# Optimization experiments

Hardware: AMD Instinct MI355X
Metric: run time of the kernel (lower is better)

## Reference

```python
import jax, jax.numpy as jnp
import numpy as np

N = 50000          # nodes
E = 800000         # edges (no self loops; self loops added in reference)
D = 128            # in_channels == out_channels (required by index_add into x)
HEADS = 1
NEG_SLOPE = 0.2
NUM_LABELS = 7


def setup_inputs() -> dict:
    key = jax.random.key(0)
    k0, k1, k2, k3, k4, k5 = jax.random.split(key, 6)
    x = jax.random.normal(k0, (N, D), dtype=jnp.float32)
    # edges guaranteed self-loop-free (remove_self_loops is then a no-op)
    src = jax.random.randint(k1, (E,), 0, N, dtype=jnp.int32)
    off = jax.random.randint(k2, (E,), 1, N, dtype=jnp.int32)
    dst = (src + off) % N
    edge_index = jnp.stack([src, dst])  # [2, E]
    node_label = jax.random.randint(k3, (N,), 0, 8, dtype=jnp.int32)  # 0 = inactive, 1..7 active
    glorot = float(np.sqrt(6.0 / (D + D)))
    weight_id = jax.random.uniform(k4, (NUM_LABELS, D, D), jnp.float32, -glorot, glorot)
    ga = float(np.sqrt(6.0 / (HEADS * 2 * D + 1)))
    att = jax.random.uniform(k5, (1, HEADS, 2 * D), jnp.float32, -ga, ga)
    return {"x": x, "edge_index": edge_index, "node_label": node_label,
            "weight_id": weight_id, "att": att}


def reference(x, edge_index, node_label, weight_id, att):
    n, d = x.shape
    # --- per-label identity transform: ox = x + W_{label-1} x for labels 1..7 ---
    y = jnp.einsum('nd,kdo->nko', x, weight_id)           # [N, 7, D]
    valid = (node_label >= 1) & (node_label <= NUM_LABELS)
    idx = jnp.clip(node_label - 1, 0, NUM_LABELS - 1)
    delta = jnp.take_along_axis(y, idx[:, None, None], axis=1)[:, 0]  # [N, D]
    ox = x + jnp.where(valid[:, None], delta, jnp.zeros_like(delta))
    # --- add self loops (input has none) ---
    loops = jnp.arange(n, dtype=edge_index.dtype)
    src = jnp.concatenate([edge_index[0], loops])
    dst = jnp.concatenate([edge_index[1], loops])
    # --- GAT message: gather, attention score, edge softmax over dst ---
    x_j = ox[src].reshape(-1, HEADS, d)                   # [Et, 1, D]
    x_i = ox[dst].reshape(-1, HEADS, d)
    alpha = (x_i * att[:, :, :d]).sum(-1) + (x_j * att[:, :, d:]).sum(-1)  # [Et, 1]
    alpha = jax.nn.leaky_relu(alpha, NEG_SLOPE)
    amax = jax.ops.segment_max(alpha, dst, num_segments=n)  # every node has a self loop
    alpha = jnp.exp(alpha - amax[dst])
    denom = jax.ops.segment_sum(alpha, dst, num_segments=n)
    alpha = alpha / (denom[dst] + 1e-16)
    # dropout p=0 (eval) -> no-op
    msg = (x_j * alpha[:, :, None]).reshape(-1, HEADS * d)  # concat=True, heads=1
    out = jax.ops.segment_sum(msg, dst, num_segments=n)     # [N, D]; bias=False
    return out
```

## Files before the change

kernel.cpp:

```cpp
#include <hip/hip_runtime.h>
#include <math.h>

#define N_NODES 50000
#define N_EDGES 800000
#define DIM 128
#define DEG_CAP 48
#define BINS ((N_NODES + 255) / 256)
#define BIN_CAP 8192
#define EA_CHUNK 3125
#define BA_BLOCKS ((N_EDGES + EA_CHUNK - 1) / EA_CHUNK)

#define LB_BLOCKS ((N_NODES + 255) / 256)
#define WT_BLOCKS ((7 * DIM * DIM + 255) / 256)
#define K1_GRID (BA_BLOCKS + LB_BLOCKS + WT_BLOCKS)

#define TR_BLOCKS 784
#define K2_GRID (BINS + TR_BLOCKS)

typedef __attribute__((ext_vector_type(8))) short short8;
typedef __attribute__((ext_vector_type(4))) float floatx4;

__device__ __forceinline__ unsigned short f2bf(float f) {
    unsigned int u = __float_as_uint(f);
    unsigned int r = (u + 0x7fff + ((u >> 16) & 1)) >> 16;
    return (unsigned short)r;
}
__device__ __forceinline__ float bf2f_lo(unsigned int v) { return __uint_as_float(v << 16); }
__device__ __forceinline__ float bf2f_hi(unsigned int v) { return __uint_as_float(v & 0xffff0000u); }

__global__ __launch_bounds__(256) void build_kernel(
        const int* __restrict__ src, const int* __restrict__ dst,
        const int* __restrict__ label, const float* __restrict__ W,
        unsigned short* __restrict__ Wt,
        int* __restrict__ bin_cur, unsigned int* __restrict__ binned,
        int* __restrict__ lab_cnt, int* __restrict__ node_list) {
    int t = threadIdx.x;
    int blk = blockIdx.x;

    if (blk < BA_BLOCKS) {
        __shared__ int hist[BINS], base_s[BINS], rank[BINS];
        for (int i = t; i < BINS; i += 256) { hist[i] = 0; rank[i] = 0; }
        __syncthreads();
        int e0 = blk * EA_CHUNK;
        int e1 = e0 + EA_CHUNK; if (e1 > N_EDGES) e1 = N_EDGES;
        for (int e = e0 + t; e < e1; e += 256) atomicAdd(&hist[dst[e] >> 8], 1);
        __syncthreads();
        for (int i = t; i < BINS; i += 256)
            base_s[i] = (hist[i] > 0) ? atomicAdd(&bin_cur[i], hist[i]) : 0;
        __syncthreads();
        for (int e = e0 + t; e < e1; e += 256) {
            int d = dst[e];
            int b = d >> 8;
            int r = atomicAdd(&rank[b], 1);
            int slot = base_s[b] + r;
            if (slot < BIN_CAP)
                binned[(size_t)b * BIN_CAP + slot] = (unsigned int)(src[e] | ((d & 255) << 16));
        }
    } else if (blk < BA_BLOCKS + LB_BLOCKS) {
        __shared__ int lcnt[8], lbase[8], lrank[8];
        int i = (blk - BA_BLOCKS) * 256 + t;
        if (t < 8) { lcnt[t] = 0; lrank[t] = 0; }
        __syncthreads();
        int b = -1;
        if (i < N_NODES) {
            int lab = label[i];
            b = (lab >= 1 && lab <= 7) ? (lab - 1) : 7;
            atomicAdd(&lcnt[b], 1);
        }
        __syncthreads();
        if (t < 8) lbase[t] = (lcnt[t] > 0) ? atomicAdd(&lab_cnt[t], lcnt[t]) : 0;
        __syncthreads();
        if (i < N_NODES) {
            int r = atomicAdd(&lrank[b], 1);
            node_list[(size_t)b * N_NODES + lbase[b] + r] = i;
        }
    } else {
        int j = (blk - BA_BLOCKS - LB_BLOCKS) * 256 + t;
        if (j < 7 * DIM * DIM) {
            int b = j >> 14;
            int d = (j >> 7) & 127;
            int c = j & 127;
            Wt[((size_t)b * DIM + c) * DIM + d] = f2bf(W[j]);
        }
    }
}

__global__ __launch_bounds__(256) void phase2_kernel(
        const float* __restrict__ x, const float* __restrict__ att,
        const int* __restrict__ lab_cnt, const int* __restrict__ node_list,
        const unsigned short* __restrict__ Wt,
        const int* __restrict__ bin_cur, const unsigned int* __restrict__ binned,
        unsigned short* __restrict__ oxh, float* __restrict__ ai, float* __restrict__ aj,
        int* __restrict__ cnt, unsigned short* __restrict__ bucket) {
    int t = threadIdx.x;
    int blk = blockIdx.x;

    if (blk < BINS) {
        __shared__ unsigned short rows[256][DEG_CAP];
        __shared__ int lcnt[256];
        int b = blk;
        int m = bin_cur[b]; if (m > BIN_CAP) m = BIN_CAP;
        const unsigned int* bp = binned + (size_t)b * BIN_CAP;

        lcnt[t] = 0;
        __syncthreads();
        for (int i = t; i < m; i += 256) {
            unsigned int v = bp[i];
            int ln = (v >> 16) & 255;
            int p = atomicAdd(&lcnt[ln], 1);
            if (p < DEG_CAP) rows[ln][p] = (unsigned short)(v & 0xFFFF);
        }
        __syncthreads();
        int n = b * 256 + t;
        if (n < N_NODES) {
            int deg = lcnt[t];
            if (deg > DEG_CAP) deg = DEG_CAP;
            cnt[n] = deg;
        }
        uint4* gdst = (uint4*)(bucket + (size_t)b * 256 * DEG_CAP);
        const uint4* lsrc = (const uint4*)rows;
        #pragma unroll
        for (int k = 0; k < (256 * DEG_CAP * 2 / 16) / 256; k++)
            gdst[t + k * 256] = lsrc[t + k * 256];
    } else {
        int wv = t >> 6;
        int lane = t & 63;
        int tile = (blk - BINS) * 4 + wv;

        int b = 0, base = 0, tcnt = 0;
        for (; b < 8; b++) {
            int c = lab_cnt[b];
            int nt = (c + 15) >> 4;
            if (tile < nt) { base = b * N_NODES + tile * 16; tcnt = c - tile * 16; break; }
            tile -= nt;
        }
        if (b == 8) return;
        if (tcnt > 16) tcnt = 16;

        int m = lane & 15;
        int quad = lane >> 4;

        floatx4 acc[8];
        #pragma unroll
        for (int nt = 0; nt < 8; nt++) acc[nt] = (floatx4){0.f, 0.f, 0.f, 0.f};

        if (b < 7) {
            int mm = (m < tcnt) ? m : 0;
            int nodeA = node_list[base + mm];
            const float* xrow = x + (size_t)nodeA * DIM;
            short8 afrag[4];
            #pragma unroll
            for (int kk = 0; kk < 4; kk++) {
                float4 f0 = *(const float4*)(xrow + kk * 32 + quad * 8);
                float4 f1 = *(const float4*)(xrow + kk * 32 + quad * 8 + 4);
                short8 a;
                a[0] = (short)f2bf(f0.x); a[1] = (short)f2bf(f0.y);
                a[2] = (short)f2bf(f0.z); a[3] = (short)f2bf(f0.w);
                a[4] = (short)f2bf(f1.x); a[5] = (short)f2bf(f1.y);
                a[6] = (short)f2bf(f1.z); a[7] = (short)f2bf(f1.w);
                afrag[kk] = a;
            }

            const unsigned short* WtB = Wt + (size_t)b * DIM * DIM;
            #pragma unroll
            for (int kk = 0; kk < 4; kk++) {
                #pragma unroll
                for (int nt = 0; nt < 8; nt++) {
                    short8 bfrag = *(const short8*)(WtB + (size_t)(nt * 16 + m) * DIM + kk * 32 + quad * 8);
                    acc[nt] = __builtin_amdgcn_mfma_f32_16x16x32_bf16(afrag[kk], bfrag, acc[nt], 0, 0, 0);
                }
            }
        }

        int nodes[4];
        #pragma unroll
        for (int r = 0; r < 4; r++) {
            int rw = quad * 4 + r;
            nodes[r] = node_list[base + ((rw < tcnt) ? rw : 0)];
        }
        float pi[4] = {0.f, 0.f, 0.f, 0.f};
        float pj[4] = {0.f, 0.f, 0.f, 0.f};
        #pragma unroll
        for (int nt = 0; nt < 8; nt++) {
            int c = nt * 16 + m;
            float a1 = att[c];
            float a2 = att[DIM + c];
            #pragma unroll
            for (int r = 0; r < 4; r++) {
                int rw = quad * 4 + r;
                if (rw < tcnt) {
                    float xv = x[(size_t)nodes[r] * DIM + c];
                    float v = (b < 7) ? (acc[nt][r] + xv) : xv;
                    oxh[(size_t)nodes[r] * DIM + c] = f2bf(v);
                    pi[r] += v * a1;
                    pj[r] += v * a2;
                }
            }
        }
        #pragma unroll
        for (int r = 0; r < 4; r++) {
            #pragma unroll
            for (int off = 1; off < 16; off <<= 1) {
                pi[r] += __shfl_xor(pi[r], off, 64);
                pj[r] += __shfl_xor(pj[r], off, 64);
            }
            int rw = quad * 4 + r;
            if (m == 0 && rw < tcnt) {
                ai[nodes[r]] = pi[r];
                aj[nodes[r]] = pj[r];
            }
        }
    }
}

__global__ __launch_bounds__(256) void gather6_kernel(
        const int* __restrict__ cnt, const unsigned short* __restrict__ bucket,
        const float* __restrict__ ai, const float* __restrict__ aj,
        const uint4* __restrict__ tab,
        float* __restrict__ out) {
    int wv = threadIdx.x >> 6;
    int lane = threadIdx.x & 63;
    int n = blockIdx.x * 4 + wv;
    if (n >= N_NODES) return;
    int deg = cnt[n];
    if (deg > DEG_CAP) deg = DEG_CAP;
    const unsigned short* row = bucket + (size_t)n * DEG_CAP;
    float ain = ai[n];

    float a = -INFINITY;
    int s = n;
    if (lane < deg) {
        s = row[lane];
        a = ain + aj[s];
        a = (a > 0.0f) ? a : 0.2f * a;
    } else if (lane == deg) {
        a = ain + aj[n];
        a = (a > 0.0f) ? a : 0.2f * a;
    }
    float mx = a;
    #pragma unroll
    for (int off = 32; off > 0; off >>= 1) mx = fmaxf(mx, __shfl_xor(mx, off, 64));
    float w = expf(a - mx);
    float ssum = w;
    #pragma unroll
    for (int off = 32; off > 0; off >>= 1) ssum += __shfl_xor(ssum, off, 64);
    float wn = w / (ssum + 1e-16f);
    float wsf = __shfl(wn, deg, 64);

    int g = lane >> 4;
    int cl = lane & 15;
    float ac0 = 0.f, ac1 = 0.f, ac2 = 0.f, ac3 = 0.f;
    float ac4 = 0.f, ac5 = 0.f, ac6 = 0.f, ac7 = 0.f;

    if (g == 0) {
        uint4 v = tab[(size_t)n * 16 + cl];
        ac0 += wsf * bf2f_lo(v.x); ac1 += wsf * bf2f_hi(v.x);
        ac2 += wsf * bf2f_lo(v.y); ac3 += wsf * bf2f_hi(v.y);
        ac4 += wsf * bf2f_lo(v.z); ac5 += wsf * bf2f_hi(v.z);
        ac6 += wsf * bf2f_lo(v.w); ac7 += wsf * bf2f_hi(v.w);
    }

    int niter = (deg + 3) >> 2;
    for (int k = 0; k < niter; k++) {
        int i = g + 4 * k;
        bool valid = (i < deg);
        int idx = valid ? i : 0;
        float wi = __shfl(wn, idx, 64);
        int   si = __shfl(s, idx, 64);
        if (!valid) wi = 0.0f;
        uint4 v = tab[(size_t)si * 16 + cl];
        ac0 += wi * bf2f_lo(v.x); ac1 += wi * bf2f_hi(v.x);
        ac2 += wi * bf2f_lo(v.y); ac3 += wi * bf2f_hi(v.y);
        ac4 += wi * bf2f_lo(v.z); ac5 += wi * bf2f_hi(v.z);
        ac6 += wi * bf2f_lo(v.w); ac7 += wi * bf2f_hi(v.w);
    }

    #pragma unroll
    for (int off = 16; off < 64; off <<= 1) {
        ac0 += __shfl_xor(ac0, off, 64); ac1 += __shfl_xor(ac1, off, 64);
        ac2 += __shfl_xor(ac2, off, 64); ac3 += __shfl_xor(ac3, off, 64);
        ac4 += __shfl_xor(ac4, off, 64); ac5 += __shfl_xor(ac5, off, 64);
        ac6 += __shfl_xor(ac6, off, 64); ac7 += __shfl_xor(ac7, off, 64);
    }
    if (g == 0) {
        float* op = out + (size_t)n * DIM + cl * 8;
        float4 o0; o0.x = ac0; o0.y = ac1; o0.z = ac2; o0.w = ac3;
        float4 o1; o1.x = ac4; o1.y = ac5; o1.z = ac6; o1.w = ac7;
        *(float4*)op = o0;
        *(float4*)(op + 4) = o1;
    }
}

extern "C" void kernel_launch(void* const* d_in, const int* in_sizes, int n_in,
                              void* d_out, int out_size, void* d_ws, size_t ws_size,
                              hipStream_t stream) {
    const float* x     = (const float*)d_in[0];
    const int*   ei    = (const int*)d_in[1];
    const int*   label = (const int*)d_in[2];
    const float* W     = (const float*)d_in[3];
    const float* att   = (const float*)d_in[4];
    float* out = (float*)d_out;

    const int* src = ei;
    const int* dst = ei + N_EDGES;

    char* w = (char*)d_ws;
    unsigned short* oxh    = (unsigned short*)w; w += sizeof(unsigned short) * (size_t)N_NODES * DIM;
    unsigned short* Wt     = (unsigned short*)w; w += sizeof(unsigned short) * 7 * DIM * DIM;
    unsigned short* bucket = (unsigned short*)w; w += sizeof(unsigned short) * (size_t)BINS * 256 * DEG_CAP;
    unsigned int*   binned = (unsigned int*)w;   w += sizeof(unsigned int) * (size_t)BINS * BIN_CAP;
    float* ai        = (float*)w;  w += sizeof(float) * N_NODES;
    float* aj        = (float*)w;  w += sizeof(float) * N_NODES;
    int*   cnt       = (int*)w;    w += sizeof(int) * N_NODES;
    int*   node_list = (int*)w;    w += sizeof(int) * (size_t)8 * N_NODES;
    int*   lab_cnt   = (int*)w;    w += sizeof(int) * 8;
    int*   bin_cur   = (int*)w;    w += sizeof(int) * BINS;

    hipMemsetAsync(lab_cnt, 0, sizeof(int) * (8 + BINS), stream);

    build_kernel<<<K1_GRID, 256, 0, stream>>>(src, dst, label, W,
                                              Wt, bin_cur, binned, lab_cnt, node_list);

    phase2_kernel<<<K2_GRID, 256, 0, stream>>>(x, att, lab_cnt, node_list, Wt,
                                               bin_cur, binned, oxh, ai, aj, cnt, bucket);

    gather6_kernel<<<(N_NODES + 3) / 4, 256, 0, stream>>>(cnt, bucket, ai, aj,
                                                          (const uint4*)oxh, out);
}
```

Measured before the change: 166.6 us.

## Split transform tiles across two waves and stage softmax weights in LDS for gather

```diff
diff --git a/kernel.cpp b/kernel.cpp
--- a/kernel.cpp
+++ b/kernel.cpp
@@ -14,7 +14,7 @@
 #define WT_BLOCKS ((7 * DIM * DIM + 255) / 256)
 #define K1_GRID (BA_BLOCKS + LB_BLOCKS + WT_BLOCKS)
 
-#define TR_BLOCKS 784
+#define TR_BLOCKS 1568
 #define K2_GRID (BINS + TR_BLOCKS)
 
 typedef __attribute__((ext_vector_type(8))) short short8;
@@ -125,7 +125,9 @@
     } else {
         int wv = t >> 6;
         int lane = t & 63;
-        int tile = (blk - BINS) * 4 + wv;
+        int gw = (blk - BINS) * 4 + wv;
+        int tile = gw >> 1;
+        int half = gw & 1;
 
         int b = 0, base = 0, tcnt = 0;
         for (; b < 8; b++) {
@@ -140,9 +142,9 @@
         int m = lane & 15;
         int quad = lane >> 4;
 
-        floatx4 acc[8];
-        #pragma unroll
-        for (int nt = 0; nt < 8; nt++) acc[nt] = (floatx4){0.f, 0.f, 0.f, 0.f};
+        floatx4 acc[4];
+        #pragma unroll
+        for (int nt = 0; nt < 4; nt++) acc[nt] = (floatx4){0.f, 0.f, 0.f, 0.f};
 
         if (b < 7) {
             int mm = (m < tcnt) ? m : 0;
@@ -165,8 +167,8 @@
             #pragma unroll
             for (int kk = 0; kk < 4; kk++) {
                 #pragma unroll
-                for (int nt = 0; nt < 8; nt++) {
-                    short8 bfrag = *(const short8*)(WtB + (size_t)(nt * 16 + m) * DIM + kk * 32 + quad * 8);
+                for (int nt = 0; nt < 4; nt++) {
+                    short8 bfrag = *(const short8*)(WtB + (size_t)(half * 64 + nt * 16 + m) * DIM + kk * 32 + quad * 8);
                     acc[nt] = __builtin_amdgcn_mfma_f32_16x16x32_bf16(afrag[kk], bfrag, acc[nt], 0, 0, 0);
                 }
             }
@@ -181,8 +183,8 @@
         float pi[4] = {0.f, 0.f, 0.f, 0.f};
         float pj[4] = {0.f, 0.f, 0.f, 0.f};
         #pragma unroll
-        for (int nt = 0; nt < 8; nt++) {
-            int c = nt * 16 + m;
+        for (int nt = 0; nt < 4; nt++) {
+            int c = half * 64 + nt * 16 + m;
             float a1 = att[c];
             float a2 = att[DIM + c];
             #pragma unroll
@@ -206,22 +208,23 @@
             }
             int rw = quad * 4 + r;
             if (m == 0 && rw < tcnt) {
-                ai[nodes[r]] = pi[r];
-                aj[nodes[r]] = pj[r];
-            }
-        }
-    }
-}
-
-__global__ __launch_bounds__(256) void gather6_kernel(
+                atomicAdd(&ai[nodes[r]], pi[r]);
+                atomicAdd(&aj[nodes[r]], pj[r]);
+            }
+        }
+    }
+}
+
+__global__ __launch_bounds__(256) void gather7_kernel(
         const int* __restrict__ cnt, const unsigned short* __restrict__ bucket,
         const float* __restrict__ ai, const float* __restrict__ aj,
         const uint4* __restrict__ tab,
         float* __restrict__ out) {
+    __shared__ float wls[4][64];
+    __shared__ int   sls[4][64];
     int wv = threadIdx.x >> 6;
     int lane = threadIdx.x & 63;
     int n = blockIdx.x * 4 + wv;
-    if (n >= N_NODES) return;
     int deg = cnt[n];
     if (deg > DEG_CAP) deg = DEG_CAP;
     const unsigned short* row = bucket + (size_t)n * DEG_CAP;
@@ -245,7 +248,14 @@
     #pragma unroll
     for (int off = 32; off > 0; off >>= 1) ssum += __shfl_xor(ssum, off, 64);
     float wn = w / (ssum + 1e-16f);
-    float wsf = __shfl(wn, deg, 64);
+
+    wls[wv][lane] = wn;
+    sls[wv][lane] = s;
+    __syncthreads();
+
+    const float* wp = wls[wv];
+    const int*   sp = sls[wv];
+    float wsf = wp[deg];
 
     int g = lane >> 4;
     int cl = lane & 15;
@@ -261,18 +271,34 @@
     }
 
     int niter = (deg + 3) >> 2;
-    for (int k = 0; k < niter; k++) {
-        int i = g + 4 * k;
-        bool valid = (i < deg);
-        int idx = valid ? i : 0;
-        float wi = __shfl(wn, idx, 64);
-        int   si = __shfl(s, idx, 64);
-        if (!valid) wi = 0.0f;
-        uint4 v = tab[(size_t)si * 16 + cl];
-        ac0 += wi * bf2f_lo(v.x); ac1 += wi * bf2f_hi(v.x);
-        ac2 += wi * bf2f_lo(v.y); ac3 += wi * bf2f_hi(v.y);
-        ac4 += wi * bf2f_lo(v.z); ac5 += wi * bf2f_hi(v.z);
-        ac6 += wi * bf2f_lo(v.w); ac7 += wi * bf2f_hi(v.w);
+    int k = 0;
+    for (; k + 2 <= niter; k += 2) {
+        int i0 = g + 4 * k;
+        int i1 = i0 + 4;
+        float w0 = wp[i0]; int s0 = sp[i0];
+        float w1 = wp[i1]; int s1 = sp[i1];
+        if (i0 >= deg) w0 = 0.0f;
+        if (i1 >= deg) w1 = 0.0f;
+        uint4 v0 = tab[(size_t)s0 * 16 + cl];
+        uint4 v1 = tab[(size_t)s1 * 16 + cl];
+        ac0 += w0 * bf2f_lo(v0.x); ac1 += w0 * bf2f_hi(v0.x);
+        ac2 += w0 * bf2f_lo(v0.y); ac3 += w0 * bf2f_hi(v0.y);
+        ac4 += w0 * bf2f_lo(v0.z); ac5 += w0 * bf2f_hi(v0.z);
+        ac6 += w0 * bf2f_lo(v0.w); ac7 += w0 * bf2f_hi(v0.w);
+        ac0 += w1 * bf2f_lo(v1.x); ac1 += w1 * bf2f_hi(v1.x);
+        ac2 += w1 * bf2f_lo(v1.y); ac3 += w1 * bf2f_hi(v1.y);
+        ac4 += w1 * bf2f_lo(v1.z); ac5 += w1 * bf2f_hi(v1.z);
+        ac6 += w1 * bf2f_lo(v1.w); ac7 += w1 * bf2f_hi(v1.w);
+    }
+    if (k < niter) {
+        int i0 = g + 4 * k;
+        float w0 = (i0 < deg) ? wp[i0] : 0.0f;
+        int s0 = sp[i0];
+        uint4 v0 = tab[(size_t)s0 * 16 + cl];
+        ac0 += w0 * bf2f_lo(v0.x); ac1 += w0 * bf2f_hi(v0.x);
+        ac2 += w0 * bf2f_lo(v0.y); ac3 += w0 * bf2f_hi(v0.y);
+        ac4 += w0 * bf2f_lo(v0.z); ac5 += w0 * bf2f_hi(v0.z);
+        ac6 += w0 * bf2f_lo(v0.w); ac7 += w0 * bf2f_hi(v0.w);
     }
 
     #pragma unroll
@@ -309,14 +335,14 @@
     unsigned short* Wt     = (unsigned short*)w; w += sizeof(unsigned short) * 7 * DIM * DIM;
     unsigned short* bucket = (unsigned short*)w; w += sizeof(unsigned short) * (size_t)BINS * 256 * DEG_CAP;
     unsigned int*   binned = (unsigned int*)w;   w += sizeof(unsigned int) * (size_t)BINS * BIN_CAP;
+    int*   cnt       = (int*)w;    w += sizeof(int) * N_NODES;
+    int*   node_list = (int*)w;    w += sizeof(int) * (size_t)8 * N_NODES;
     float* ai        = (float*)w;  w += sizeof(float) * N_NODES;
     float* aj        = (float*)w;  w += sizeof(float) * N_NODES;
-    int*   cnt       = (int*)w;    w += sizeof(int) * N_NODES;
-    int*   node_list = (int*)w;    w += sizeof(int) * (size_t)8 * N_NODES;
     int*   lab_cnt   = (int*)w;    w += sizeof(int) * 8;
     int*   bin_cur   = (int*)w;    w += sizeof(int) * BINS;
 
-    hipMemsetAsync(lab_cnt, 0, sizeof(int) * (8 + BINS), stream);
+    hipMemsetAsync(ai, 0, sizeof(float) * 2 * N_NODES + sizeof(int) * (8 + BINS), stream);
 
     build_kernel<<<K1_GRID, 256, 0, stream>>>(src, dst, label, W,
                                               Wt, bin_cur, binned, lab_cnt, node_list);
@@ -324,6 +350,6 @@
     phase2_kernel<<<K2_GRID, 256, 0, stream>>>(x, att, lab_cnt, node_list, Wt,
                                                bin_cur, binned, oxh, ai, aj, cnt, bucket);
 
-    gather6_kernel<<<(N_NODES + 3) / 4, 256, 0, stream>>>(cnt, bucket, ai, aj,
+    gather7_kernel<<<(N_NODES + 3) / 4, 256, 0, stream>>>(cnt, bucket, ai, aj,
                                                           (const uint4*)oxh, out);
 }
```

Result: no change. 169.0 us (+1.5%).
